# Performance work log

Hardware: AMD Instinct MI355X
Metric: run time of the kernel (lower is better)

The kernel has to match this reference:

```python
import jax, jax.numpy as jnp
import numpy as np

DIM = 512
FEAT = 64
BATCH = 2048

def setup_inputs() -> dict:
    key = jax.random.key(0)
    kx, kw, kb = jax.random.split(key, 3)
    x = jax.random.normal(kx, (BATCH, DIM, FEAT), dtype=jnp.float32)
    # torch Linear weight is [out, in]; emulate Kaiming-uniform-ish init scale
    bound = 1.0 / np.sqrt(FEAT)
    W = jax.random.uniform(kw, (DIM, FEAT, FEAT), dtype=jnp.float32, minval=-bound, maxval=bound)
    b = jax.random.uniform(kb, (DIM, FEAT), dtype=jnp.float32, minval=-bound, maxval=bound)
    return {"x": x, "W": W, "b": b}

def reference(x, W, b):
    # per-slice Linear: out[:, d, :] = x[:, d, :] @ W[d].T + b[d]
    # fused as one batched contraction over the feature (input) axis 'f'
    return jnp.einsum('bdf,dgf->bdg', x, W) + b[None, :, :]
```

## Files before the change

### kernel.cpp

```cpp
#include <hip/hip_runtime.h>
#include <hip/hip_bf16.h>

#define DIM  512
#define FEAT 64
#define BATCH 2048

#define D_PER_BLOCK 64
#define NITER 16

using bf16x8 = __attribute__((ext_vector_type(8))) short;
using f32x4  = __attribute__((ext_vector_type(4))) float;

__device__ inline short f2bf(float f) {
    unsigned int u = __float_as_uint(f);
    u += 0x7fffu + ((u >> 16) & 1u);
    return (short)(u >> 16);
}

__device__ inline bf16x8 cvt8(float4 a, float4 b) {
    bf16x8 r;
    r[0] = f2bf(a.x); r[1] = f2bf(a.y); r[2] = f2bf(a.z); r[3] = f2bf(a.w);
    r[4] = f2bf(b.x); r[5] = f2bf(b.y); r[6] = f2bf(b.z); r[7] = f2bf(b.w);
    return r;
}

__global__ __launch_bounds__(256)
void w_prep(const float* __restrict__ W, short* __restrict__ ws) {
    const int d = blockIdx.x;
    const int t = threadIdx.x;
    const int l = t & 63, g0 = t >> 6;
#pragma unroll
    for (int h = 0; h < 2; ++h) {
        const int g8 = g0 + h * 4;
        const int mt = g8 & 3, ks = g8 >> 2;
        const float* src = W + ((size_t)d * FEAT + mt * 16 + (l & 15)) * FEAT
                             + ks * 32 + (l >> 4) * 8;
        float4 w0 = *(const float4*)src;
        float4 w1 = *(const float4*)(src + 4);
        *(bf16x8*)(ws + ((size_t)(d * 8 + g8) * 64 + l) * 8) = cvt8(w0, w1);
    }
}

template<bool PRE>
__global__ __launch_bounds__(256, 2)
void split_linear_main(const float* __restrict__ x,
                       const float* __restrict__ W,
                       const short* __restrict__ Wb,
                       const float* __restrict__ bias,
                       float* __restrict__ out)
{
    __shared__ float obuf[4][1024];

    const int id = blockIdx.x;
    const int dq = id & 7;
    const int rt = id >> 3;
    const int d0 = dq * D_PER_BLOCK;
    const int b0 = rt * 16;

    const int tid  = threadIdx.x;
    const int wave = tid >> 6;
    const int lane = tid & 63;
    const int lr   = lane & 15;
    const int lk   = lane >> 4;

    const int dw = d0 + wave;

    const float* xp  = x    + ((size_t)(b0 + lr) * DIM + dw) * FEAT + lk * 8;
    const float* bp  = bias + (size_t)dw * FEAT + lr * 4;
    const short* wbp = Wb   + (size_t)dw * 4096 + lane * 8;
    float*       opb = out  + ((size_t)b0 * DIM + dw) * FEAT + lr * 4;
    float* sl = &obuf[wave][0];

    float4 xc[4], xn[4];
    f32x4 bc, bn;

    auto LOADX = [&](float4* xr, int i) {
        const float* xq = xp + (size_t)i * 256;
        xr[0] = *(const float4*)(xq);
        xr[1] = *(const float4*)(xq + 4);
        xr[2] = *(const float4*)(xq + 32);
        xr[3] = *(const float4*)(xq + 36);
    };
    auto LOADB = [&](int i) -> f32x4 {
        return *(const f32x4*)(bp + (size_t)i * 256);
    };

    auto BODY = [&](float4* xr, f32x4 bv, int i) {
        bf16x8 wf[8];
        if (PRE) {
            const short* wq = wbp + (size_t)i * 16384;
#pragma unroll
            for (int g = 0; g < 8; ++g)
                wf[g] = *(const bf16x8*)(wq + g * 512);
        } else {
            const float* wq = W + ((size_t)(dw + i * 4) * FEAT) * FEAT;
#pragma unroll
            for (int g = 0; g < 8; ++g) {
                const int mt = g & 3, ks = g >> 2;
                const float* p = wq + ((size_t)(mt * 16 + lr)) * FEAT + ks * 32 + lk * 8;
                float4 a = *(const float4*)p;
                float4 b = *(const float4*)(p + 4);
                wf[g] = cvt8(a, b);
            }
        }

        bf16x8 af0 = cvt8(xr[0], xr[1]);
        bf16x8 af1 = cvt8(xr[2], xr[3]);

        f32x4 acc[4] = {{0.f,0.f,0.f,0.f},{0.f,0.f,0.f,0.f},
                        {0.f,0.f,0.f,0.f},{0.f,0.f,0.f,0.f}};
#pragma unroll
        for (int mt = 0; mt < 4; ++mt)
            acc[mt] = __builtin_amdgcn_mfma_f32_16x16x32_bf16(wf[mt],     af0, acc[mt], 0, 0, 0);
#pragma unroll
        for (int mt = 0; mt < 4; ++mt)
            acc[mt] = __builtin_amdgcn_mfma_f32_16x16x32_bf16(wf[4 + mt], af1, acc[mt], 0, 0, 0);

#pragma unroll
        for (int mt = 0; mt < 4; ++mt) {
            const int c  = mt * 4 + lk;
            const int pc = c ^ (lr & 7);
            *(f32x4*)&sl[lr * 64 + pc * 4] = acc[mt];
        }

#pragma unroll
        for (int j = 0; j < 4; ++j) {
            const int rr  = j * 4 + lk;
            const int pc2 = lr ^ (rr & 7);
            f32x4 v = *(const f32x4*)&sl[rr * 64 + pc2 * 4];
            v += bv;
            __builtin_nontemporal_store(v,
                (f32x4*)(opb + (size_t)rr * (DIM * FEAT) + (size_t)i * 256));
        }
    };

    LOADX(xc, 0); bc = LOADB(0);
    for (int i = 0; i < NITER; i += 2) {
        LOADX(xn, i + 1); bn = LOADB(i + 1);
        BODY(xc, bc, i);
        if (i + 2 < NITER) { LOADX(xc, i + 2); bc = LOADB(i + 2); }
        BODY(xn, bn, i + 1);
    }
}

extern "C" void kernel_launch(void* const* d_in, const int* in_sizes, int n_in,
                              void* d_out, int out_size, void* d_ws, size_t ws_size,
                              hipStream_t stream) {
    const float* x    = (const float*)d_in[0];
    const float* W    = (const float*)d_in[1];
    const float* bias = (const float*)d_in[2];
    float* out        = (float*)d_out;

    const size_t WSNEED = (size_t)DIM * 8 * 64 * 8 * sizeof(short);
    dim3 block(256, 1, 1);
    dim3 grid((BATCH / 16) * (DIM / D_PER_BLOCK), 1, 1);

    if (ws_size >= WSNEED) {
        short* ws = (short*)d_ws;
        w_prep<<<dim3(DIM), block, 0, stream>>>(W, ws);
        split_linear_main<true><<<grid, block, 0, stream>>>(x, nullptr, ws, bias, out);
    } else {
        split_linear_main<false><<<grid, block, 0, stream>>>(x, W, nullptr, bias, out);
    }
}
```

Baseline: 129.1 us.

## Stage x tiles into LDS via async global_load_lds with double buffering

Replaces the per-wave register prefetch of x with async global-to-LDS loads into a two-slot LDS ring, staged two tiles ahead and XOR-swizzled. Each block now loads a whole 16-row by 4-dim tile so that every row reads a contiguous 1 KB run of x. W fragments are prefetched one tile ahead in registers. The output is transposed through the same LDS slot so stores are row-contiguous. In exchange it adds explicit vmcnt waits and several block-wide barriers per tile, which serialise the waves and depend on hand-counted wait values being correct.

```diff
diff --git a/kernel.cpp b/kernel.cpp
--- a/kernel.cpp
+++ b/kernel.cpp
@@ -5,11 +5,14 @@
 #define FEAT 64
 #define BATCH 2048
 
-#define D_PER_BLOCK 64
-#define NITER 16
+#define DPB    64
+#define NTILES 16
 
 using bf16x8 = __attribute__((ext_vector_type(8))) short;
 using f32x4  = __attribute__((ext_vector_type(4))) float;
+
+typedef __attribute__((address_space(3))) float lds_f;
+typedef __attribute__((address_space(1))) const float glb_f;
 
 __device__ inline short f2bf(float f) {
     unsigned int u = __float_as_uint(f);
@@ -35,9 +38,8 @@
         const int mt = g8 & 3, ks = g8 >> 2;
         const float* src = W + ((size_t)d * FEAT + mt * 16 + (l & 15)) * FEAT
                              + ks * 32 + (l >> 4) * 8;
-        float4 w0 = *(const float4*)src;
-        float4 w1 = *(const float4*)(src + 4);
-        *(bf16x8*)(ws + ((size_t)(d * 8 + g8) * 64 + l) * 8) = cvt8(w0, w1);
+        *(bf16x8*)(ws + ((size_t)(d * 8 + g8) * 64 + l) * 8)
+            = cvt8(*(const float4*)src, *(const float4*)(src + 4));
     }
 }
 
@@ -49,13 +51,13 @@
                        const float* __restrict__ bias,
                        float* __restrict__ out)
 {
-    __shared__ float obuf[4][1024];
+    __shared__ float slot[2][16][256];
 
     const int id = blockIdx.x;
-    const int dq = id & 7;
-    const int rt = id >> 3;
-    const int d0 = dq * D_PER_BLOCK;
-    const int b0 = rt * 16;
+    const int dc = id & 7;
+    const int rc = id >> 3;
+    const int d0 = dc * DPB;
+    const int b0 = rc * 16;
 
     const int tid  = threadIdx.x;
     const int wave = tid >> 6;
@@ -63,83 +65,109 @@
     const int lr   = lane & 15;
     const int lk   = lane >> 4;
 
-    const int dw = d0 + wave;
-
-    const float* xp  = x    + ((size_t)(b0 + lr) * DIM + dw) * FEAT + lk * 8;
-    const float* bp  = bias + (size_t)dw * FEAT + lr * 4;
-    const short* wbp = Wb   + (size_t)dw * 4096 + lane * 8;
-    float*       opb = out  + ((size_t)b0 * DIM + dw) * FEAT + lr * 4;
-    float* sl = &obuf[wave][0];
-
-    float4 xc[4], xn[4];
-    f32x4 bc, bn;
-
-    auto LOADX = [&](float4* xr, int i) {
-        const float* xq = xp + (size_t)i * 256;
-        xr[0] = *(const float4*)(xq);
-        xr[1] = *(const float4*)(xq + 4);
-        xr[2] = *(const float4*)(xq + 32);
-        xr[3] = *(const float4*)(xq + 36);
-    };
-    auto LOADB = [&](int i) -> f32x4 {
-        return *(const f32x4*)(bp + (size_t)i * 256);
+    auto stage = [&](int s, int t) {
+#pragma unroll
+        for (int i = 0; i < 4; ++i) {
+            const int r = wave * 4 + i;
+            const float* gp = x + ((size_t)(b0 + r) * DIM + d0 + t * 4) * FEAT
+                                + (lane >> 4) * 64 + (((lane & 15) ^ (r & 7)) << 2);
+            __builtin_amdgcn_global_load_lds((glb_f*)gp, (lds_f*)&slot[s][r][0], 16, 0, 0);
+        }
     };
 
-    auto BODY = [&](float4* xr, f32x4 bv, int i) {
-        bf16x8 wf[8];
+    const short* wbp = Wb + ((size_t)(d0 + wave)) * 4096 + lane * 8;
+    const float* bsp = bias + (size_t)d0 * FEAT + lane * 4;
+
+    auto LOADW = [&](bf16x8 (&wf)[8], f32x4& bv, int t) {
         if (PRE) {
-            const short* wq = wbp + (size_t)i * 16384;
+            const short* wq = wbp + (size_t)t * 4 * 4096;
 #pragma unroll
             for (int g = 0; g < 8; ++g)
                 wf[g] = *(const bf16x8*)(wq + g * 512);
         } else {
-            const float* wq = W + ((size_t)(dw + i * 4) * FEAT) * FEAT;
+            const float* wq = W + (size_t)(d0 + t * 4 + wave) * FEAT * FEAT;
 #pragma unroll
             for (int g = 0; g < 8; ++g) {
                 const int mt = g & 3, ks = g >> 2;
-                const float* p = wq + ((size_t)(mt * 16 + lr)) * FEAT + ks * 32 + lk * 8;
-                float4 a = *(const float4*)p;
-                float4 b = *(const float4*)(p + 4);
-                wf[g] = cvt8(a, b);
+                const float* p = wq + (size_t)(mt * 16 + lr) * FEAT + ks * 32 + lk * 8;
+                wf[g] = cvt8(*(const float4*)p, *(const float4*)(p + 4));
             }
         }
+        bv = *(const f32x4*)(bsp + t * 256);
+    };
 
-        bf16x8 af0 = cvt8(xr[0], xr[1]);
-        bf16x8 af1 = cvt8(xr[2], xr[3]);
+    auto BODY = [&](bf16x8 (&wfc)[8], bf16x8 (&wfn)[8], f32x4& bvc, f32x4& bvn, int t) {
+        const int s = t & 1;
+        if (t == 0 || t == NTILES - 1)
+            asm volatile("s_waitcnt vmcnt(4)" ::: "memory");
+        else
+            asm volatile("s_waitcnt vmcnt(8)" ::: "memory");
+        __builtin_amdgcn_s_barrier();
+        __builtin_amdgcn_sched_barrier(0);
+
+        if (t + 1 < NTILES) LOADW(wfn, bvn, t + 1);
+
+        const float* sl = &slot[s][0][0];
+        const int rbase = lr * 256 + wave * 64;
+        float4 p0a = *(const float4*)&sl[rbase + (((lk * 2 + 0) ^ (lr & 7)) << 2)];
+        float4 p0b = *(const float4*)&sl[rbase + (((lk * 2 + 1) ^ (lr & 7)) << 2)];
+        float4 p1a = *(const float4*)&sl[rbase + (((8 + lk * 2 + 0) ^ (lr & 7)) << 2)];
+        float4 p1b = *(const float4*)&sl[rbase + (((8 + lk * 2 + 1) ^ (lr & 7)) << 2)];
+
+        bf16x8 af0 = cvt8(p0a, p0b);
+        bf16x8 af1 = cvt8(p1a, p1b);
 
         f32x4 acc[4] = {{0.f,0.f,0.f,0.f},{0.f,0.f,0.f,0.f},
                         {0.f,0.f,0.f,0.f},{0.f,0.f,0.f,0.f}};
 #pragma unroll
         for (int mt = 0; mt < 4; ++mt)
-            acc[mt] = __builtin_amdgcn_mfma_f32_16x16x32_bf16(wf[mt],     af0, acc[mt], 0, 0, 0);
+            acc[mt] = __builtin_amdgcn_mfma_f32_16x16x32_bf16(wfc[mt],     af0, acc[mt], 0, 0, 0);
 #pragma unroll
         for (int mt = 0; mt < 4; ++mt)
-            acc[mt] = __builtin_amdgcn_mfma_f32_16x16x32_bf16(wf[4 + mt], af1, acc[mt], 0, 0, 0);
+            acc[mt] = __builtin_amdgcn_mfma_f32_16x16x32_bf16(wfc[4 + mt], af1, acc[mt], 0, 0, 0);
 
+        asm volatile("s_waitcnt lgkmcnt(0)" ::: "memory");
+        __builtin_amdgcn_s_barrier();
+        __builtin_amdgcn_sched_barrier(0);
+
+        float* slw = &slot[s][0][0];
 #pragma unroll
         for (int mt = 0; mt < 4; ++mt) {
-            const int c  = mt * 4 + lk;
-            const int pc = c ^ (lr & 7);
-            *(f32x4*)&sl[lr * 64 + pc * 4] = acc[mt];
+            const int pc = (mt * 4 + lk) ^ (lr & 7);
+            *(f32x4*)&slw[lr * 256 + wave * 64 + pc * 4] = acc[mt];
         }
+        asm volatile("s_waitcnt lgkmcnt(0)" ::: "memory");
+        __builtin_amdgcn_s_barrier();
+        __builtin_amdgcn_sched_barrier(0);
 
 #pragma unroll
         for (int j = 0; j < 4; ++j) {
-            const int rr  = j * 4 + lk;
-            const int pc2 = lr ^ (rr & 7);
-            f32x4 v = *(const f32x4*)&sl[rr * 64 + pc2 * 4];
-            v += bv;
+            const int r = wave * 4 + j;
+            f32x4 v = *(const f32x4*)&slw[r * 256 + (lane >> 4) * 64
+                                          + (((lane & 15) ^ (r & 7)) << 2)];
+            v += bvc;
             __builtin_nontemporal_store(v,
-                (f32x4*)(opb + (size_t)rr * (DIM * FEAT) + (size_t)i * 256));
+                (f32x4*)(out + ((size_t)(b0 + r) * DIM + d0 + t * 4) * FEAT + lane * 4));
         }
+        __builtin_amdgcn_sched_barrier(0);
+        if (t + 2 < NTILES) stage(s, t + 2);
+        __builtin_amdgcn_sched_barrier(0);
     };
 
-    LOADX(xc, 0); bc = LOADB(0);
-    for (int i = 0; i < NITER; i += 2) {
-        LOADX(xn, i + 1); bn = LOADB(i + 1);
-        BODY(xc, bc, i);
-        if (i + 2 < NITER) { LOADX(xc, i + 2); bc = LOADB(i + 2); }
-        BODY(xn, bn, i + 1);
+    bf16x8 wfA[8], wfB[8];
+    f32x4 bvA, bvB;
+
+    stage(0, 0);
+    __builtin_amdgcn_sched_barrier(0);
+    LOADW(wfA, bvA, 0);
+    __builtin_amdgcn_sched_barrier(0);
+    stage(1, 1);
+    __builtin_amdgcn_sched_barrier(0);
+
+#pragma unroll
+    for (int t = 0; t < NTILES; t += 2) {
+        BODY(wfA, wfB, bvA, bvB, t);
+        BODY(wfB, wfA, bvB, bvA, t + 1);
     }
 }
 
@@ -153,7 +181,7 @@
 
     const size_t WSNEED = (size_t)DIM * 8 * 64 * 8 * sizeof(short);
     dim3 block(256, 1, 1);
-    dim3 grid((BATCH / 16) * (DIM / D_PER_BLOCK), 1, 1);
+    dim3 grid((BATCH / 16) * (DIM / DPB), 1, 1);
 
     if (ws_size >= WSNEED) {
         short* ws = (short*)d_ws;
```

After: 120.6 us. 6.6% less time.
